# Kernel optimization log

Hardware: AMD Instinct MI355X
Metric: run time of the kernel (lower is better)

The kernel has to match this reference:

```python
import jax, jax.numpy as jnp
import numpy as np

B, T, U, V = 8, 128, 100, 1024
BLANK = 0
NEG = -1e30  # safe -inf surrogate (finite grads through logaddexp)


def setup_inputs() -> dict:
    key = jax.random.key(0)
    k1, k2 = jax.random.split(key)
    logits = jax.random.normal(k1, (B, T, U + 1, V), dtype=jnp.float32)
    # targets drawn from non-blank ids [1, V)
    targets = jax.random.randint(k2, (B, U), 1, V, dtype=jnp.int32)
    logit_lengths = jnp.full((B,), T, dtype=jnp.int32)
    target_lengths = jnp.full((B,), U, dtype=jnp.int32)
    return {"logits": logits, "targets": targets,
            "logit_lengths": logit_lengths, "target_lengths": target_lengths}


def _rnnt_nll(log_probs, targets, t_len, u_len):
    """Negative log-likelihood of one utterance.
    log_probs: [T, U+1, V] (log-softmaxed joiner output), targets: [U] int.
    alpha[t,u] = logaddexp(alpha[t-1,u] + blank[t-1,u], alpha[t,u-1] + emit[t,u-1]).
    """
    blank_lp = log_probs[:, :, BLANK]                      # [T, U+1]
    emit_lp = log_probs[:, jnp.arange(U), targets]         # [T, U]

    # row t=0: pure emissions
    alpha0 = jnp.concatenate([jnp.zeros((1,), log_probs.dtype),
                              jnp.cumsum(emit_lp[0])])     # [U+1]

    def combine(x, y):
        # linear log-space recurrence x[u] = logaddexp(c[u], x[u-1] + a[u])
        a1, c1 = x
        a2, c2 = y
        return (a1 + a2, jnp.logaddexp(c2, c1 + a2))

    def step(prev_row, inp):
        blank_prev, emit_t = inp                           # [U+1], [U]
        c = prev_row + blank_prev                          # vertical (blank) moves
        a = jnp.concatenate([jnp.full((1,), NEG, log_probs.dtype), emit_t])
        _, row = jax.lax.associative_scan(combine, (a, c))
        return row, row

    _, rows = jax.lax.scan(step, alpha0, (blank_lp[:-1], emit_lp[1:]))
    alpha = jnp.concatenate([alpha0[None, :], rows], axis=0)  # [T, U+1]

    ll = alpha[t_len - 1, u_len] + blank_lp[t_len - 1, u_len]
    return -ll


def reference(logits, targets, logit_lengths, target_lengths):
    log_probs = jax.nn.log_softmax(logits, axis=-1)
    # module passes src_lengths - 1 to rnnt_loss
    t_lens = logit_lengths - 1
    nll = jax.vmap(_rnnt_nll)(log_probs, targets, t_lens, target_lengths)
    return jnp.mean(nll)  # reduction='mean'
```

## Files before the change

kernel.cpp:

```cpp
#include <hip/hip_runtime.h>


#define NEGV (-1e30f)

constexpr int Bb = 8;
constexpr int Tt = 128;
constexpr int Uu = 100;
constexpr int Vv = 1024;
constexpr int UP1 = Uu + 1;
constexpr int NSTEP = 232;
constexpr int DROWS = 244;
constexpr int DPAD  = 104;

__device__ __forceinline__ float laddexp(float x, float y) {
    float m = fmaxf(x, y);
    float d = fabsf(x - y);
    return m + __logf(1.0f + __expf(-d));
}

__device__ __forceinline__ float wave_shr1(float x) {
    return __builtin_bit_cast(float, __builtin_amdgcn_update_dpp(
        0, __builtin_bit_cast(int, x), 0x138, 0xf, 0xf, true));
}

__device__ __forceinline__ float readlane_f(float x, int lane) {
    return __builtin_bit_cast(float,
        __builtin_amdgcn_readlane(__builtin_bit_cast(int, x), lane));
}

__global__ __launch_bounds__(256) void lse_kernel(
        const float* __restrict__ logits,
        const int*   __restrict__ targets,
        float* __restrict__ bS,
        float* __restrict__ eS) {
    const int wid  = blockIdx.x * 4 + (threadIdx.x >> 6);
    const int lane = threadIdx.x & 63;
    const int b   = wid / (Tt * UP1);
    const int rem = wid - b * (Tt * UP1);
    const int t   = rem / UP1;
    const int u   = rem - t * UP1;

    const float* row = logits + (size_t)wid * Vv;
    const float4* r4 = (const float4*)row;
    float4 x0 = r4[lane];
    float4 x1 = r4[lane + 64];
    float4 x2 = r4[lane + 128];
    float4 x3 = r4[lane + 192];

    float m = fmaxf(fmaxf(fmaxf(x0.x, x0.y), fmaxf(x0.z, x0.w)),
                    fmaxf(fmaxf(x1.x, x1.y), fmaxf(x1.z, x1.w)));
    m = fmaxf(m, fmaxf(fmaxf(fmaxf(x2.x, x2.y), fmaxf(x2.z, x2.w)),
                       fmaxf(fmaxf(x3.x, x3.y), fmaxf(x3.z, x3.w))));
    #pragma unroll
    for (int d = 32; d > 0; d >>= 1) m = fmaxf(m, __shfl_xor(m, d, 64));

    float s = __expf(x0.x - m) + __expf(x0.y - m) + __expf(x0.z - m) + __expf(x0.w - m)
            + __expf(x1.x - m) + __expf(x1.y - m) + __expf(x1.z - m) + __expf(x1.w - m)
            + __expf(x2.x - m) + __expf(x2.y - m) + __expf(x2.z - m) + __expf(x2.w - m)
            + __expf(x3.x - m) + __expf(x3.y - m) + __expf(x3.z - m) + __expf(x3.w - m);
    #pragma unroll
    for (int d = 32; d > 0; d >>= 1) s += __shfl_xor(s, d, 64);

    float lse = m + __logf(s);

    if (lane == 0) {
        const int dw = t + u + 1;
        bS[((size_t)b * DROWS + dw) * DPAD + u] = x0.x - lse;
        if (u < Uu) {
            int tgt = targets[b * Uu + u];
            eS[((size_t)b * DROWS + dw) * DPAD + (u + 1)] = row[tgt] - lse;
        }
    }
}

__global__ __launch_bounds__(64) void dp_kernel(
        const float* __restrict__ bS,
        const float* __restrict__ eS,
        const int*   __restrict__ logit_lengths,
        const int*   __restrict__ target_lengths,
        float* __restrict__ nll) {
    const int b    = blockIdx.x;
    const int lane = threadIdx.x;
    const float* bB = bS + (size_t)b * DROWS * DPAD;
    const float* eB = eS + (size_t)b * DROWS * DPAD;
    const int tl = logit_lengths[b];
    const int ul = target_lengths[b];
    const int t_idx = tl - 2;
    const int dcap  = t_idx + ul;

    const int u0 = lane * 2, u1 = u0 + 1;

    float aP0 = (lane == 0) ? 0.0f : NEGV;
    float aP1 = NEGV;
    float cap = (dcap == 0) ? 0.0f : NEGV;

    const float* pb = bB + DPAD + u0;
    const float* pe = eB + DPAD + u0;

    float2 B0 = *(const float2*)(pb + 0*DPAD), E0 = *(const float2*)(pe + 0*DPAD);
    float2 B1 = *(const float2*)(pb + 1*DPAD), E1 = *(const float2*)(pe + 1*DPAD);
    float2 B2 = *(const float2*)(pb + 2*DPAD), E2 = *(const float2*)(pe + 2*DPAD);
    float2 B3 = *(const float2*)(pb + 3*DPAD), E3 = *(const float2*)(pe + 3*DPAD);
    float2 B4 = *(const float2*)(pb + 4*DPAD), E4 = *(const float2*)(pe + 4*DPAD);
    float2 B5 = *(const float2*)(pb + 5*DPAD), E5 = *(const float2*)(pe + 5*DPAD);
    float2 B6 = *(const float2*)(pb + 6*DPAD), E6 = *(const float2*)(pe + 6*DPAD);
    float2 B7 = *(const float2*)(pb + 7*DPAD), E7 = *(const float2*)(pe + 7*DPAD);

    const float* pbL = pb + 8*DPAD;
    const float* peL = pe + 8*DPAD;

    int dv = 1;
#define STEP(Bq, Eq) do {                                              \
        float sh  = wave_shr1(aP1);                                    \
        float t1b = (u1 < dv) ? aP1 + Bq.y : NEGV;                     \
        float t1e = aP0 + Eq.y;                                        \
        float t0b = (u0 < dv) ? aP0 + Bq.x : NEGV;                     \
        float t0e = (lane >= 1) ? sh + Eq.x : NEGV;                    \
        float n1 = laddexp(t1b, t1e);                                  \
        float n0 = laddexp(t0b, t0e);                                  \
        Bq = *(const float2*)pbL; Eq = *(const float2*)peL;            \
        pbL += DPAD; peL += DPAD;                                      \
        aP0 = n0; aP1 = n1;                                            \
        if (dv == dcap) {                                              \
            float w0 = readlane_f(n0, ul >> 1);                        \
            float w1 = readlane_f(n1, ul >> 1);                        \
            cap = (ul & 1) ? w1 : w0;                                  \
        }                                                              \
        ++dv;                                                          \
    } while (0)

    for (int it = 0; it < NSTEP / 8; ++it) {
        STEP(B0, E0); STEP(B1, E1); STEP(B2, E2); STEP(B3, E3);
        STEP(B4, E4); STEP(B5, E5); STEP(B6, E6); STEP(B7, E7);
    }
#undef STEP

    if (lane == 0) {
        float ll = cap + bB[(size_t)(dcap + 1) * DPAD + ul];
        nll[b] = -ll;
    }
}

__global__ void mean_kernel(const float* __restrict__ nll, float* __restrict__ out) {
    if (threadIdx.x == 0 && blockIdx.x == 0) {
        float s = 0.0f;
        for (int i = 0; i < Bb; ++i) s += nll[i];
        out[0] = s / (float)Bb;
    }
}

extern "C" void kernel_launch(void* const* d_in, const int* in_sizes, int n_in,
                              void* d_out, int out_size, void* d_ws, size_t ws_size,
                              hipStream_t stream) {
    const float* logits         = (const float*)d_in[0];
    const int*   targets        = (const int*)d_in[1];
    const int*   logit_lengths  = (const int*)d_in[2];
    const int*   target_lengths = (const int*)d_in[3];
    float* out = (float*)d_out;

    float* ws = (float*)d_ws;
    float* bS = ws;
    float* eS = bS + (size_t)Bb * DROWS * DPAD;
    float* nll = eS + (size_t)Bb * DROWS * DPAD;

    const int rows = Bb * Tt * UP1;
    lse_kernel<<<rows / 4, 256, 0, stream>>>(logits, targets, bS, eS);
    dp_kernel<<<Bb, 64, 0, stream>>>(bS, eS, logit_lengths, target_lengths, nll);
    mean_kernel<<<1, 64, 0, stream>>>(nll, out);
}
```

Measured before the change: 109.2 us.

## Split DP kernel into producer wave prefetching into LDS ring and compute wave

The anti-diagonal DP kernel now uses two waves per batch. One wave streams chunks of blank/emit log-prob rows from global memory into a double-buffered LDS ring while the other runs the recurrence out of LDS. This is meant to hide global load latency on the serial DP chain. In exchange it adds a block barrier every chunk and LDS round-trips, which may cost more than the latency it hides.

New measurement: 106.3 us. -2.6%, faster.

```diff
diff --git a/kernel.cpp b/kernel.cpp
--- a/kernel.cpp
+++ b/kernel.cpp
@@ -8,9 +8,10 @@
 constexpr int Uu = 100;
 constexpr int Vv = 1024;
 constexpr int UP1 = Uu + 1;
-constexpr int NSTEP = 232;
 constexpr int DROWS = 244;
 constexpr int DPAD  = 104;
+constexpr int CHUNK = 8;
+constexpr int LPITCH = 128;
 
 __device__ __forceinline__ float laddexp(float x, float y) {
     float m = fmaxf(x, y);
@@ -73,14 +74,16 @@
     }
 }
 
-__global__ __launch_bounds__(64) void dp_kernel(
+__global__ __launch_bounds__(128) void dp_kernel(
         const float* __restrict__ bS,
         const float* __restrict__ eS,
         const int*   __restrict__ logit_lengths,
         const int*   __restrict__ target_lengths,
         float* __restrict__ nll) {
     const int b    = blockIdx.x;
-    const int lane = threadIdx.x;
+    const int tid  = threadIdx.x;
+    const int wv   = tid >> 6;
+    const int lane = tid & 63;
     const float* bB = bS + (size_t)b * DROWS * DPAD;
     const float* eB = eS + (size_t)b * DROWS * DPAD;
     const int tl = logit_lengths[b];
@@ -88,57 +91,94 @@
     const int t_idx = tl - 2;
     const int dcap  = t_idx + ul;
 
+    __shared__ float ringB[2][CHUNK][LPITCH];
+    __shared__ float ringE[2][CHUNK][LPITCH];
+
     const int u0 = lane * 2, u1 = u0 + 1;
-
     float aP0 = (lane == 0) ? 0.0f : NEGV;
     float aP1 = NEGV;
     float cap = (dcap == 0) ? 0.0f : NEGV;
 
-    const float* pb = bB + DPAD + u0;
-    const float* pe = eB + DPAD + u0;
-
-    float2 B0 = *(const float2*)(pb + 0*DPAD), E0 = *(const float2*)(pe + 0*DPAD);
-    float2 B1 = *(const float2*)(pb + 1*DPAD), E1 = *(const float2*)(pe + 1*DPAD);
-    float2 B2 = *(const float2*)(pb + 2*DPAD), E2 = *(const float2*)(pe + 2*DPAD);
-    float2 B3 = *(const float2*)(pb + 3*DPAD), E3 = *(const float2*)(pe + 3*DPAD);
-    float2 B4 = *(const float2*)(pb + 4*DPAD), E4 = *(const float2*)(pe + 4*DPAD);
-    float2 B5 = *(const float2*)(pb + 5*DPAD), E5 = *(const float2*)(pe + 5*DPAD);
-    float2 B6 = *(const float2*)(pb + 6*DPAD), E6 = *(const float2*)(pe + 6*DPAD);
-    float2 B7 = *(const float2*)(pb + 7*DPAD), E7 = *(const float2*)(pe + 7*DPAD);
-
-    const float* pbL = pb + 8*DPAD;
-    const float* peL = pe + 8*DPAD;
-
-    int dv = 1;
-#define STEP(Bq, Eq) do {                                              \
-        float sh  = wave_shr1(aP1);                                    \
-        float t1b = (u1 < dv) ? aP1 + Bq.y : NEGV;                     \
-        float t1e = aP0 + Eq.y;                                        \
-        float t0b = (u0 < dv) ? aP0 + Bq.x : NEGV;                     \
-        float t0e = (lane >= 1) ? sh + Eq.x : NEGV;                    \
-        float n1 = laddexp(t1b, t1e);                                  \
-        float n0 = laddexp(t0b, t0e);                                  \
-        Bq = *(const float2*)pbL; Eq = *(const float2*)peL;            \
-        pbL += DPAD; peL += DPAD;                                      \
-        aP0 = n0; aP1 = n1;                                            \
-        if (dv == dcap) {                                              \
-            float w0 = readlane_f(n0, ul >> 1);                        \
-            float w1 = readlane_f(n1, ul >> 1);                        \
-            cap = (ul & 1) ? w1 : w0;                                  \
-        }                                                              \
-        ++dv;                                                          \
+    float2 LAb[CHUNK], LAe[CHUNK], LBb[CHUNK], LBe[CHUNK];
+
+#define PLOAD(SETb, SETe, ck) do {                                           \
+        const float* _pb = bB + (size_t)((ck) * CHUNK + 1) * DPAD + lane * 2;\
+        const float* _pe = eB + (size_t)((ck) * CHUNK + 1) * DPAD + lane * 2;\
+        _Pragma("unroll")                                                    \
+        for (int r = 0; r < CHUNK; ++r) {                                    \
+            SETb[r] = *(const float2*)(_pb + r * DPAD);                      \
+            SETe[r] = *(const float2*)(_pe + r * DPAD);                      \
+        }                                                                    \
     } while (0)
 
-    for (int it = 0; it < NSTEP / 8; ++it) {
-        STEP(B0, E0); STEP(B1, E1); STEP(B2, E2); STEP(B3, E3);
-        STEP(B4, E4); STEP(B5, E5); STEP(B6, E6); STEP(B7, E7);
-    }
-#undef STEP
-
-    if (lane == 0) {
-        float ll = cap + bB[(size_t)(dcap + 1) * DPAD + ul];
-        nll[b] = -ll;
-    }
+#define PWRITE(SETb, SETe, slot) do {                                        \
+        _Pragma("unroll")                                                    \
+        for (int r = 0; r < CHUNK; ++r) {                                    \
+            *(float2*)&ringB[slot][r][lane * 2] = SETb[r];                   \
+            *(float2*)&ringE[slot][r][lane * 2] = SETe[r];                   \
+        }                                                                    \
+    } while (0)
+
+#define CCHUNK(cc, slot) do {                                                \
+        float2 Bv[CHUNK], Ev[CHUNK];                                         \
+        _Pragma("unroll")                                                    \
+        for (int r = 0; r < CHUNK; ++r) {                                    \
+            Bv[r] = *(const float2*)&ringB[slot][r][u0];                     \
+            Ev[r] = *(const float2*)&ringE[slot][r][u0];                     \
+        }                                                                    \
+        _Pragma("unroll")                                                    \
+        for (int r = 0; r < CHUNK; ++r) {                                    \
+            const int dv = (cc) * CHUNK + 1 + r;                             \
+            float sh  = wave_shr1(aP1);                                      \
+            float t1b = (u1 < dv) ? aP1 + Bv[r].y : NEGV;                    \
+            float t1e = aP0 + Ev[r].y;                                       \
+            float t0b = (u0 < dv) ? aP0 + Bv[r].x : NEGV;                    \
+            float t0e = (lane >= 1) ? sh + Ev[r].x : NEGV;                   \
+            float n1 = laddexp(t1b, t1e);                                    \
+            float n0 = laddexp(t0b, t0e);                                    \
+            aP0 = n0; aP1 = n1;                                              \
+            if (dv == dcap) {                                                \
+                float w0 = readlane_f(n0, ul >> 1);                          \
+                float w1 = readlane_f(n1, ul >> 1);                          \
+                cap = (ul & 1) ? w1 : w0;                                    \
+            }                                                                \
+        }                                                                    \
+    } while (0)
+
+    if (wv == 1) {
+        PLOAD(LAb, LAe, 0);
+        PLOAD(LBb, LBe, 1);
+        PWRITE(LAb, LAe, 0);
+    }
+    __syncthreads();
+
+    for (int c2 = 0; c2 < 14; ++c2) {
+        const int c = c2 * 2;
+        if (wv == 1) {
+            PLOAD(LAb, LAe, c + 2);
+            PWRITE(LBb, LBe, 1);
+        } else {
+            CCHUNK(c, 0);
+        }
+        __syncthreads();
+        if (wv == 1) {
+            if (c2 < 13) PLOAD(LBb, LBe, c + 3);
+            PWRITE(LAb, LAe, 0);
+        } else {
+            CCHUNK(c + 1, 1);
+        }
+        __syncthreads();
+    }
+    if (wv == 0) {
+        CCHUNK(28, 0);
+        if (lane == 0) {
+            float ll = cap + bB[(size_t)(dcap + 1) * DPAD + ul];
+            nll[b] = -ll;
+        }
+    }
+#undef PLOAD
+#undef PWRITE
+#undef CCHUNK
 }
 
 __global__ void mean_kernel(const float* __restrict__ nll, float* __restrict__ out) {
@@ -158,13 +198,13 @@
     const int*   target_lengths = (const int*)d_in[3];
     float* out = (float*)d_out;
 
-    float* ws = (float*)d_ws;
-    float* bS = ws;
-    float* eS = bS + (size_t)Bb * DROWS * DPAD;
+    float* ws  = (float*)d_ws;
+    float* bS  = ws;
+    float* eS  = bS + (size_t)Bb * DROWS * DPAD;
     float* nll = eS + (size_t)Bb * DROWS * DPAD;
 
     const int rows = Bb * Tt * UP1;
     lse_kernel<<<rows / 4, 256, 0, stream>>>(logits, targets, bS, eS);
-    dp_kernel<<<Bb, 64, 0, stream>>>(bS, eS, logit_lengths, target_lengths, nll);
+    dp_kernel<<<Bb, 128, 0, stream>>>(bS, eS, logit_lengths, target_lengths, nll);
     mean_kernel<<<1, 64, 0, stream>>>(nll, out);
 }
```

## Stage DP inputs in LDS via producer waves with flags, store as fp16

Applied to the files above, without the earlier changes.

Stores the blank and emit log-probs as half precision instead of float. The DP kernel now has eight producer waves that copy diagonal regions into LDS and signal through workgroup-scope flags, while a single consumer wave runs the recurrence out of shared memory. The aim is to take global-load latency off the serial DP critical path and halve the intermediate traffic. In exchange, fp16 rounding of log-probs loses precision, and the consumer adds spin-wait overhead.

New measurement: 112.7 us. +3.3%, slower.

```diff
diff --git a/kernel.cpp b/kernel.cpp
--- a/kernel.cpp
+++ b/kernel.cpp
@@ -1,4 +1,5 @@
 #include <hip/hip_runtime.h>
+#include <hip/hip_fp16.h>
 
 
 #define NEGV (-1e30f)
@@ -8,9 +9,11 @@
 constexpr int Uu = 100;
 constexpr int Vv = 1024;
 constexpr int UP1 = Uu + 1;
-constexpr int NSTEP = 232;
 constexpr int DROWS = 244;
 constexpr int DPAD  = 104;
+constexpr int LROWS = 233;
+constexpr int REG   = 29;
+constexpr int NREG  = 8;
 
 __device__ __forceinline__ float laddexp(float x, float y) {
     float m = fmaxf(x, y);
@@ -31,8 +34,8 @@
 __global__ __launch_bounds__(256) void lse_kernel(
         const float* __restrict__ logits,
         const int*   __restrict__ targets,
-        float* __restrict__ bS,
-        float* __restrict__ eS) {
+        __half* __restrict__ bS,
+        __half* __restrict__ eS) {
     const int wid  = blockIdx.x * 4 + (threadIdx.x >> 6);
     const int lane = threadIdx.x & 63;
     const int b   = wid / (Tt * UP1);
@@ -65,79 +68,93 @@
 
     if (lane == 0) {
         const int dw = t + u + 1;
-        bS[((size_t)b * DROWS + dw) * DPAD + u] = x0.x - lse;
+        bS[((size_t)b * DROWS + dw) * DPAD + u] = __float2half(x0.x - lse);
         if (u < Uu) {
             int tgt = targets[b * Uu + u];
-            eS[((size_t)b * DROWS + dw) * DPAD + (u + 1)] = row[tgt] - lse;
+            eS[((size_t)b * DROWS + dw) * DPAD + (u + 1)] = __float2half(row[tgt] - lse);
         }
     }
 }
 
-__global__ __launch_bounds__(64) void dp_kernel(
-        const float* __restrict__ bS,
-        const float* __restrict__ eS,
-        const int*   __restrict__ logit_lengths,
-        const int*   __restrict__ target_lengths,
+__global__ __launch_bounds__(576) void dp_kernel(
+        const __half* __restrict__ bS,
+        const __half* __restrict__ eS,
+        const int*    __restrict__ logit_lengths,
+        const int*    __restrict__ target_lengths,
         float* __restrict__ nll) {
     const int b    = blockIdx.x;
-    const int lane = threadIdx.x;
-    const float* bB = bS + (size_t)b * DROWS * DPAD;
-    const float* eB = eS + (size_t)b * DROWS * DPAD;
+    const int tid  = threadIdx.x;
+    const int wvi  = tid >> 6;
+    const int lane = tid & 63;
+
+    __shared__ __align__(16) __half lB[LROWS][DPAD];
+    __shared__ __align__(16) __half lE[LROWS][DPAD];
+    __shared__ int sflag[NREG];
+
+    if (tid < NREG) sflag[tid] = 0;
+    __syncthreads();
+
+    const size_t bstride = (size_t)DROWS * DPAD;
+
+    if (wvi >= 1) {
+        const int w = wvi - 1;
+        const int row0 = 1 + REG * w;
+        constexpr int RBYTES = REG * DPAD * 2;
+        const char* gb = (const char*)(bS + (size_t)b * bstride + (size_t)row0 * DPAD);
+        const char* ge = (const char*)(eS + (size_t)b * bstride + (size_t)row0 * DPAD);
+        char* db = (char*)&lB[row0][0];
+        char* de = (char*)&lE[row0][0];
+        for (int k = lane * 16; k < RBYTES; k += 64 * 16) {
+            *(uint4*)(db + k) = *(const uint4*)(gb + k);
+            *(uint4*)(de + k) = *(const uint4*)(ge + k);
+        }
+        __hip_atomic_store(&sflag[w], 1, __ATOMIC_RELEASE,
+                           __HIP_MEMORY_SCOPE_WORKGROUP);
+        return;
+    }
+
     const int tl = logit_lengths[b];
     const int ul = target_lengths[b];
     const int t_idx = tl - 2;
     const int dcap  = t_idx + ul;
 
     const int u0 = lane * 2, u1 = u0 + 1;
-
     float aP0 = (lane == 0) ? 0.0f : NEGV;
     float aP1 = NEGV;
     float cap = (dcap == 0) ? 0.0f : NEGV;
 
-    const float* pb = bB + DPAD + u0;
-    const float* pe = eB + DPAD + u0;
+    for (int w = 0; w < NREG; ++w) {
+        while (__hip_atomic_load(&sflag[w], __ATOMIC_ACQUIRE,
+                                 __HIP_MEMORY_SCOPE_WORKGROUP) == 0)
+            __builtin_amdgcn_s_sleep(1);
+        __builtin_amdgcn_sched_barrier(0);
 
-    float2 B0 = *(const float2*)(pb + 0*DPAD), E0 = *(const float2*)(pe + 0*DPAD);
-    float2 B1 = *(const float2*)(pb + 1*DPAD), E1 = *(const float2*)(pe + 1*DPAD);
-    float2 B2 = *(const float2*)(pb + 2*DPAD), E2 = *(const float2*)(pe + 2*DPAD);
-    float2 B3 = *(const float2*)(pb + 3*DPAD), E3 = *(const float2*)(pe + 3*DPAD);
-    float2 B4 = *(const float2*)(pb + 4*DPAD), E4 = *(const float2*)(pe + 4*DPAD);
-    float2 B5 = *(const float2*)(pb + 5*DPAD), E5 = *(const float2*)(pe + 5*DPAD);
-    float2 B6 = *(const float2*)(pb + 6*DPAD), E6 = *(const float2*)(pe + 6*DPAD);
-    float2 B7 = *(const float2*)(pb + 7*DPAD), E7 = *(const float2*)(pe + 7*DPAD);
-
-    const float* pbL = pb + 8*DPAD;
-    const float* peL = pe + 8*DPAD;
-
-    int dv = 1;
-#define STEP(Bq, Eq) do {                                              \
-        float sh  = wave_shr1(aP1);                                    \
-        float t1b = (u1 < dv) ? aP1 + Bq.y : NEGV;                     \
-        float t1e = aP0 + Eq.y;                                        \
-        float t0b = (u0 < dv) ? aP0 + Bq.x : NEGV;                     \
-        float t0e = (lane >= 1) ? sh + Eq.x : NEGV;                    \
-        float n1 = laddexp(t1b, t1e);                                  \
-        float n0 = laddexp(t0b, t0e);                                  \
-        Bq = *(const float2*)pbL; Eq = *(const float2*)peL;            \
-        pbL += DPAD; peL += DPAD;                                      \
-        aP0 = n0; aP1 = n1;                                            \
-        if (dv == dcap) {                                              \
-            float w0 = readlane_f(n0, ul >> 1);                        \
-            float w1 = readlane_f(n1, ul >> 1);                        \
-            cap = (ul & 1) ? w1 : w0;                                  \
-        }                                                              \
-        ++dv;                                                          \
-    } while (0)
-
-    for (int it = 0; it < NSTEP / 8; ++it) {
-        STEP(B0, E0); STEP(B1, E1); STEP(B2, E2); STEP(B3, E3);
-        STEP(B4, E4); STEP(B5, E5); STEP(B6, E6); STEP(B7, E7);
+        const int dbase = 1 + REG * w;
+        for (int j = 0; j < REG; ++j) {
+            const int dv = dbase + j;
+            const __half2 hB = *(const __half2*)&lB[dv][u0];
+            const __half2 hE = *(const __half2*)&lE[dv][u0];
+            const float2 Bf = __half22float2(hB);
+            const float2 Ef = __half22float2(hE);
+            float sh  = wave_shr1(aP1);
+            float t1b = (u1 < dv) ? aP1 + Bf.y : NEGV;
+            float t1e = aP0 + Ef.y;
+            float t0b = (u0 < dv) ? aP0 + Bf.x : NEGV;
+            float t0e = (lane >= 1) ? sh + Ef.x : NEGV;
+            float n1 = laddexp(t1b, t1e);
+            float n0 = laddexp(t0b, t0e);
+            aP0 = n0; aP1 = n1;
+            if (dv == dcap) {
+                float w0 = readlane_f(n0, ul >> 1);
+                float w1 = readlane_f(n1, ul >> 1);
+                cap = (ul & 1) ? w1 : w0;
+            }
+        }
     }
-#undef STEP
 
     if (lane == 0) {
-        float ll = cap + bB[(size_t)(dcap + 1) * DPAD + ul];
-        nll[b] = -ll;
+        float blk = __half2float(lB[dcap + 1][ul]);
+        nll[b] = -(cap + blk);
     }
 }
 
@@ -158,13 +175,12 @@
     const int*   target_lengths = (const int*)d_in[3];
     float* out = (float*)d_out;
 
-    float* ws = (float*)d_ws;
-    float* bS = ws;
-    float* eS = bS + (size_t)Bb * DROWS * DPAD;
-    float* nll = eS + (size_t)Bb * DROWS * DPAD;
+    __half* bS = (__half*)d_ws;
+    __half* eS = bS + (size_t)Bb * DROWS * DPAD;
+    float*  nll = (float*)(eS + (size_t)Bb * DROWS * DPAD);
 
     const int rows = Bb * Tt * UP1;
     lse_kernel<<<rows / 4, 256, 0, stream>>>(logits, targets, bS, eS);
-    dp_kernel<<<Bb, 64, 0, stream>>>(bS, eS, logit_lengths, target_lengths, nll);
+    dp_kernel<<<Bb, 576, 0, stream>>>(bS, eS, logit_lengths, target_lengths, nll);
     mean_kernel<<<1, 64, 0, stream>>>(nll, out);
 }
```
